# Kernel optimization log

Measured on AMD Instinct MI355X. Metric: run time of the kernel, lower is better.

The kernel has to match this reference:

```python
import jax, jax.numpy as jnp
import numpy as np

B, A, C, M = 4, 120000, 80, 32
ALPHA, GAMMA, EPS = 0.75, 2.0, 1e-4
STD = np.array([0.1, 0.1, 0.2, 0.2, 0.1, 0.1, 0.2, 0.2], dtype=np.float32)


def _make_boxes(key, shape, img=1024.0):
    k1, k2, k3, k4 = jax.random.split(key, 4)
    cx = jax.random.uniform(k1, shape) * img
    cy = jax.random.uniform(k2, shape) * img
    w = jax.random.uniform(k3, shape) * 224.0 + 32.0
    h = jax.random.uniform(k4, shape) * 224.0 + 32.0
    return jnp.stack([cx - 0.5 * w, cy - 0.5 * h, cx + 0.5 * w, cy + 0.5 * h], axis=-1)


def setup_inputs() -> dict:
    key = jax.random.key(0)
    kc, kr, ka, kh, kf, kl, ki = jax.random.split(key, 7)
    classifications = jax.random.uniform(kc, (B, A, C), dtype=jnp.float32)
    regressions = jax.random.normal(kr, (B, A, 8), dtype=jnp.float32)
    anchors = _make_boxes(ka, (1, A))  # [1,A,4]
    head = _make_boxes(kh, (B, M))     # [B,M,4]
    full = _make_boxes(kf, (B, M))     # [B,M,4]
    labels = jax.random.randint(kl, (B, M, 1), 0, C).astype(jnp.float32)
    ignore = jax.random.randint(ki, (B, M, 1), 0, 2).astype(jnp.float32)
    annotations = jnp.concatenate([head, full, labels, ignore], axis=-1)  # [B,M,10]
    return {"classifications": classifications, "regressions": regressions,
            "anchors": anchors, "annotations": annotations}


def _calc_iou(a, b):
    # a: [A,4], b: [B,M,4] -> [B,A,M]
    area_b = (b[..., 2] - b[..., 0]) * (b[..., 3] - b[..., 1])  # [B,M]
    a = a[None, :, None, :]
    bb = b[:, None, :, :]
    iw = jnp.clip(jnp.minimum(a[..., 2], bb[..., 2]) - jnp.maximum(a[..., 0], bb[..., 0]), 0.0)
    ih = jnp.clip(jnp.minimum(a[..., 3], bb[..., 3]) - jnp.maximum(a[..., 1], bb[..., 1]), 0.0)
    area_a = ((a[..., 2] - a[..., 0]) * (a[..., 3] - a[..., 1]))  # [1,A,1]
    inter = iw * ih
    ua = jnp.clip(area_a + area_b[:, None, :] - inter, 1e-8)
    return inter / ua


def reference(classifications, regressions, anchors, annotations):
    anchor = anchors[0]                       # [A,4]
    aw = anchor[:, 2] - anchor[:, 0]
    ah = anchor[:, 3] - anchor[:, 1]
    acx = anchor[:, 0] + 0.5 * aw
    acy = anchor[:, 1] + 0.5 * ah

    ann = annotations[..., :-1]               # [B,M,9]
    full_box = ann[..., 4:8]

    iou = _calc_iou(anchor, full_box)         # [B,A,M]
    iou_max = jnp.max(iou, axis=-1)           # [B,A]
    iou_arg = jnp.argmax(iou, axis=-1)        # [B,A]

    pos = iou_max >= 0.5                      # [B,A]
    neg = iou_max < 0.4
    num_pos = jnp.sum(pos, axis=1).astype(jnp.float32)  # [B]

    assigned = jnp.take_along_axis(ann, iou_arg[..., None], axis=1)  # [B,A,9]
    assigned_cls = assigned[..., 8].astype(jnp.int32)                # [B,A]

    one_hot = jax.nn.one_hot(assigned_cls, classifications.shape[-1], dtype=jnp.float32)
    targets = jnp.where(pos[..., None], one_hot,
                        jnp.where(neg[..., None], 0.0, -1.0))        # [B,A,C]

    p = jnp.clip(classifications, EPS, 1.0 - EPS)
    alpha_f = jnp.where(targets == 1.0, ALPHA, 1.0 - ALPHA)
    focal_w = alpha_f * jnp.where(targets == 1.0, 1.0 - p, p) ** GAMMA
    bce = -(targets * jnp.log(p) + (1.0 - targets) * jnp.log(1.0 - p))
    cls_loss = jnp.where(targets != -1.0, focal_w * bce, 0.0)
    cls_losses = jnp.sum(cls_loss, axis=(1, 2)) / jnp.clip(num_pos, 1.0)  # [B]

    gw_h = assigned[..., 2] - assigned[..., 0]
    gh_h = assigned[..., 3] - assigned[..., 1]
    gcx_h = assigned[..., 0] + 0.5 * gw_h
    gcy_h = assigned[..., 1] + 0.5 * gh_h
    gw_f = assigned[..., 6] - assigned[..., 4]
    gh_f = assigned[..., 7] - assigned[..., 5]
    gcx_f = assigned[..., 4] + 0.5 * gw_f
    gcy_f = assigned[..., 5] + 0.5 * gh_f
    gw_h = jnp.clip(gw_h, 1.0); gh_h = jnp.clip(gh_h, 1.0)
    gw_f = jnp.clip(gw_f, 1.0); gh_f = jnp.clip(gh_f, 1.0)

    t = jnp.stack([
        (gcx_f - acx) / aw, (gcy_f - acy) / ah,
        jnp.log(gw_f / aw), jnp.log(gh_f / ah),
        (gcx_h - acx) / aw * 4.0, (gcy_h - acy) / ah * 4.0,
        jnp.log(gw_h / aw * 4.0), jnp.log(gh_h / ah * 4.0),
    ], axis=-1) / jnp.asarray(STD)            # [B,A,8]

    diff = jnp.abs(t - regressions)
    # only_full=True: weights zero out cols 4:8
    diff = diff * jnp.asarray([1., 1., 1., 1., 0., 0., 0., 0.], dtype=jnp.float32)
    rl = jnp.where(diff <= 1.0 / 9.0, 0.5 * 9.0 * diff * diff, diff - 0.5 / 9.0)
    rl4 = rl[..., 0:4] * pos[..., None]       # [B,A,4], only positive anchors
    reg_losses = jnp.where(num_pos > 0,
                           jnp.sum(rl4, axis=(1, 2)) / (jnp.clip(num_pos, 1.0) * 4.0),
                           0.0)               # mean over positive rows x 4 cols

    return (jnp.mean(cls_losses, keepdims=True), jnp.mean(reg_losses, keepdims=True))
```

## Files before the change

### kernel.cpp

```cpp
#include <hip/hip_runtime.h>

#define NB 4
#define NA 120000
#define NC 80
#define NM 32

#define ALPHA_ 0.75f
#define EPS_   1e-4f
#define LN2_   0.69314718055994531f

constexpr int BLOCK = 192;
constexpr int APB   = 192;
constexpr int F4_PER_ANCHOR = NC / 4;
constexpr int P2_ITERS = APB * F4_PER_ANCHOR / BLOCK;

__device__ __forceinline__ float wave_reduce(float v) {
    #pragma unroll
    for (int off = 32; off > 0; off >>= 1) v += __shfl_down(v, off, 64);
    return v;
}

__device__ __forceinline__ float flog2(float x) { return __builtin_amdgcn_logf(x); }

__global__ __launch_bounds__(BLOCK)
void focal_main(const float* __restrict__ cls,
                const float* __restrict__ reg,
                const float* __restrict__ anchors,
                const float* __restrict__ ann,
                double* __restrict__ acc)
{
    __shared__ float s_ann[NM * 10];
    __shared__ float s_coef[APB];
    __shared__ float s_red[3][3];

    const int b   = blockIdx.y;
    const int a0  = blockIdx.x * APB;
    const int tid = threadIdx.x;

    const float4 an = ((const float4*)anchors)[a0 + tid];

    const float* annB = ann + b * NM * 10;
    const float av0 = annB[tid];
    const float av1 = (tid < NM * 10 - BLOCK) ? annB[BLOCK + tid] : 0.0f;

    const float4* cls4 = (const float4*)(cls + (size_t)b * NA * NC) + (size_t)a0 * F4_PER_ANCHOR;
    float4 x[P2_ITERS];
    #pragma unroll
    for (int it = 0; it < P2_ITERS; ++it)
        x[it] = cls4[it * BLOCK + tid];

    s_ann[tid] = av0;
    if (tid < NM * 10 - BLOCK) s_ann[BLOCK + tid] = av1;
    __syncthreads();

    float regLoss = 0.0f;
    float posCnt  = 0.0f;
    float clsCorr = 0.0f;
    const int a = a0 + tid;

    {
        const float ax1 = an.x, ay1 = an.y, ax2 = an.z, ay2 = an.w;
        const float aw  = ax2 - ax1, ah = ay2 - ay1;
        const float acx = ax1 + 0.5f * aw, acy = ay1 + 0.5f * ah;
        const float areaA = aw * ah;

        float best = -1.0f;
        int   arg  = 0;
        #pragma unroll
        for (int m = 0; m < NM; ++m) {
            const float bx1 = s_ann[m * 10 + 4];
            const float by1 = s_ann[m * 10 + 5];
            const float bx2 = s_ann[m * 10 + 6];
            const float by2 = s_ann[m * 10 + 7];
            float iw = fminf(ax2, bx2) - fmaxf(ax1, bx1); iw = fmaxf(iw, 0.0f);
            float ih = fminf(ay2, by2) - fmaxf(ay1, by1); ih = fmaxf(ih, 0.0f);
            const float inter = iw * ih;
            const float areaB = (bx2 - bx1) * (by2 - by1);
            const float ua    = fmaxf(areaA + areaB - inter, 1e-8f);
            const float iou   = inter / ua;
            if (iou > best) { best = iou; arg = m; }
        }

        const bool pos = best >= 0.5f;
        const bool neg = best < 0.4f;
        s_coef[tid] = (pos || neg) ? (-0.25f * LN2_) : 0.0f;

        if (pos) {
            posCnt = 1.0f;
            const int c = (int)s_ann[arg * 10 + 8];
            const float xc = cls[((size_t)b * NA + a) * NC + c];
            const float p  = fminf(fmaxf(xc, EPS_), 1.0f - EPS_);
            const float q  = 1.0f - p;
            const float posT = 0.75f * q * q * (-LN2_ * flog2(p));
            const float negT = 0.25f * p * p * (-LN2_ * flog2(q));
            clsCorr = posT - negT;

            const float fx1 = s_ann[arg * 10 + 4];
            const float fy1 = s_ann[arg * 10 + 5];
            const float fx2 = s_ann[arg * 10 + 6];
            const float fy2 = s_ann[arg * 10 + 7];
            float gw = fx2 - fx1, gh = fy2 - fy1;
            const float gcx = fx1 + 0.5f * gw, gcy = fy1 + 0.5f * gh;
            gw = fmaxf(gw, 1.0f); gh = fmaxf(gh, 1.0f);
            const float t0 = ((gcx - acx) / aw) * 10.0f;
            const float t1 = ((gcy - acy) / ah) * 10.0f;
            const float t2 = (LN2_ * flog2(gw / aw)) * 5.0f;
            const float t3 = (LN2_ * flog2(gh / ah)) * 5.0f;
            const float4 r4 = ((const float4*)reg)[(size_t)(b * NA + a) * 2];
            const float d0 = fabsf(t0 - r4.x);
            const float d1 = fabsf(t1 - r4.y);
            const float d2 = fabsf(t2 - r4.z);
            const float d3 = fabsf(t3 - r4.w);
            const float beta = 1.0f / 9.0f;
            #define SL1(d) ((d) <= beta ? 4.5f * (d) * (d) : (d) - 0.5f / 9.0f)
            regLoss = SL1(d0) + SL1(d1) + SL1(d2) + SL1(d3);
            #undef SL1
        }
    }
    __syncthreads();

    float clsSum = clsCorr;
    #pragma unroll
    for (int it = 0; it < P2_ITERS; ++it) {
        const int idx = it * BLOCK + tid;
        const float C = s_coef[idx / F4_PER_ANCHOR];
        const float4 x4 = x[it];

        float p0 = fminf(fmaxf(x4.x, EPS_), 1.0f - EPS_);
        float p1 = fminf(fmaxf(x4.y, EPS_), 1.0f - EPS_);
        float p2 = fminf(fmaxf(x4.z, EPS_), 1.0f - EPS_);
        float p3 = fminf(fmaxf(x4.w, EPS_), 1.0f - EPS_);

        float t0 = p0 * p0 * flog2(1.0f - p0);
        float t1 = p1 * p1 * flog2(1.0f - p1);
        float t2 = p2 * p2 * flog2(1.0f - p2);
        float t3 = p3 * p3 * flog2(1.0f - p3);

        clsSum = fmaf((t0 + t1) + (t2 + t3), C, clsSum);
    }

    const int wave = tid >> 6, lane = tid & 63;
    float rc = wave_reduce(clsSum);
    float rr = wave_reduce(regLoss);
    float rp = wave_reduce(posCnt);
    if (lane == 0) { s_red[0][wave] = rc; s_red[1][wave] = rr; s_red[2][wave] = rp; }
    __syncthreads();
    if (tid == 0) {
        float c = s_red[0][0] + s_red[0][1] + s_red[0][2];
        float r = s_red[1][0] + s_red[1][1] + s_red[1][2];
        float p = s_red[2][0] + s_red[2][1] + s_red[2][2];
        atomicAdd(&acc[b * 3 + 0], (double)c);
        atomicAdd(&acc[b * 3 + 1], (double)r);
        atomicAdd(&acc[b * 3 + 2], (double)p);
    }
}

__global__ void focal_finalize(const double* __restrict__ acc, float* __restrict__ out) {
    double clsTot = 0.0, regTot = 0.0;
    #pragma unroll
    for (int b = 0; b < NB; ++b) {
        const double np  = acc[b * 3 + 2];
        const double npc = np < 1.0 ? 1.0 : np;
        clsTot += acc[b * 3 + 0] / npc;
        regTot += (np > 0.0) ? acc[b * 3 + 1] / (npc * 4.0) : 0.0;
    }
    out[0] = (float)(clsTot / NB);
    out[1] = (float)(regTot / NB);
}

extern "C" void kernel_launch(void* const* d_in, const int* in_sizes, int n_in,
                              void* d_out, int out_size, void* d_ws, size_t ws_size,
                              hipStream_t stream) {
    const float* cls     = (const float*)d_in[0];
    const float* reg     = (const float*)d_in[1];
    const float* anchors = (const float*)d_in[2];
    const float* ann     = (const float*)d_in[3];
    float* out = (float*)d_out;
    double* acc = (double*)d_ws;

    hipMemsetAsync(acc, 0, NB * 3 * sizeof(double), stream);

    dim3 grid(NA / APB, NB);
    focal_main<<<grid, BLOCK, 0, stream>>>(cls, reg, anchors, ann, acc);
    focal_finalize<<<1, 1, 0, stream>>>(acc, out);
}
```

Before: 259.0 us.

## Shrink per-block anchor tile, bin global atomics, and parallelize finalize reduction

Blocks now cover 64 anchors with 256 threads, so there are three times as many blocks. Only the first wave does the IoU matching, and all threads load the classification tile after the matching phase. Per-block partial sums go to 64 spread-out atomic bins per accumulator instead of a single address, which cuts atomic contention. The finalize kernel now reduces those bins with wave shuffles across 768 threads. The cls loads no longer overlap the IoU loop inside a block, so the design relies on higher occupancy to hide memory latency.

```diff
diff --git a/kernel.cpp b/kernel.cpp
--- a/kernel.cpp
+++ b/kernel.cpp
@@ -5,16 +5,20 @@
 #define NC 80
 #define NM 32
 
-#define ALPHA_ 0.75f
 #define EPS_   1e-4f
 #define LN2_   0.69314718055994531f
 
-constexpr int BLOCK = 192;
-constexpr int APB   = 192;
-constexpr int F4_PER_ANCHOR = NC / 4;
-constexpr int P2_ITERS = APB * F4_PER_ANCHOR / BLOCK;
+constexpr int BLOCK = 256;
+constexpr int APB   = 64;
+constexpr int U     = 5;
+constexpr int BINS  = 64;
 
-__device__ __forceinline__ float wave_reduce(float v) {
+__device__ __forceinline__ float wave_reduce_f(float v) {
+    #pragma unroll
+    for (int off = 32; off > 0; off >>= 1) v += __shfl_down(v, off, 64);
+    return v;
+}
+__device__ __forceinline__ double wave_reduce_d(double v) {
     #pragma unroll
     for (int off = 32; off > 0; off >>= 1) v += __shfl_down(v, off, 64);
     return v;
@@ -23,42 +27,33 @@
 __device__ __forceinline__ float flog2(float x) { return __builtin_amdgcn_logf(x); }
 
 __global__ __launch_bounds__(BLOCK)
-void focal_main(const float* __restrict__ cls,
-                const float* __restrict__ reg,
-                const float* __restrict__ anchors,
-                const float* __restrict__ ann,
-                double* __restrict__ acc)
+void focal_fused(const float* __restrict__ cls,
+                 const float* __restrict__ reg,
+                 const float* __restrict__ anchors,
+                 const float* __restrict__ ann,
+                 double* __restrict__ acc)
 {
     __shared__ float s_ann[NM * 10];
     __shared__ float s_coef[APB];
-    __shared__ float s_red[3][3];
+    __shared__ float s_red[4];
+    __shared__ float s_rp[2];
 
     const int b   = blockIdx.y;
     const int a0  = blockIdx.x * APB;
     const int tid = threadIdx.x;
 
-    const float4 an = ((const float4*)anchors)[a0 + tid];
-
     const float* annB = ann + b * NM * 10;
-    const float av0 = annB[tid];
-    const float av1 = (tid < NM * 10 - BLOCK) ? annB[BLOCK + tid] : 0.0f;
-
-    const float4* cls4 = (const float4*)(cls + (size_t)b * NA * NC) + (size_t)a0 * F4_PER_ANCHOR;
-    float4 x[P2_ITERS];
-    #pragma unroll
-    for (int it = 0; it < P2_ITERS; ++it)
-        x[it] = cls4[it * BLOCK + tid];
-
-    s_ann[tid] = av0;
-    if (tid < NM * 10 - BLOCK) s_ann[BLOCK + tid] = av1;
+    if (tid < NM * 10 - BLOCK) s_ann[BLOCK + tid] = annB[BLOCK + tid];
+    s_ann[tid] = annB[tid];
     __syncthreads();
 
     float regLoss = 0.0f;
     float posCnt  = 0.0f;
     float clsCorr = 0.0f;
-    const int a = a0 + tid;
 
-    {
+    if (tid < APB) {
+        const int a = a0 + tid;
+        const float4 an = ((const float4*)anchors)[a];
         const float ax1 = an.x, ay1 = an.y, ax2 = an.z, ay2 = an.w;
         const float aw  = ax2 - ax1, ah = ay2 - ay1;
         const float acx = ax1 + 0.5f * aw, acy = ay1 + 0.5f * ah;
@@ -119,12 +114,19 @@
     }
     __syncthreads();
 
+    const float4* base4 = (const float4*)(cls + (size_t)b * NA * NC) + (size_t)a0 * (NC / 4);
+
+    float4 x[U];
+    #pragma unroll
+    for (int j = 0; j < U; ++j)
+        x[j] = base4[j * BLOCK + tid];
+
     float clsSum = clsCorr;
     #pragma unroll
-    for (int it = 0; it < P2_ITERS; ++it) {
-        const int idx = it * BLOCK + tid;
-        const float C = s_coef[idx / F4_PER_ANCHOR];
-        const float4 x4 = x[it];
+    for (int j = 0; j < U; ++j) {
+        const int idx = j * BLOCK + tid;
+        const float C = s_coef[idx / (NC / 4)];
+        const float4 x4 = x[j];
 
         float p0 = fminf(fmaxf(x4.x, EPS_), 1.0f - EPS_);
         float p1 = fminf(fmaxf(x4.y, EPS_), 1.0f - EPS_);
@@ -140,32 +142,43 @@
     }
 
     const int wave = tid >> 6, lane = tid & 63;
-    float rc = wave_reduce(clsSum);
-    float rr = wave_reduce(regLoss);
-    float rp = wave_reduce(posCnt);
-    if (lane == 0) { s_red[0][wave] = rc; s_red[1][wave] = rr; s_red[2][wave] = rp; }
+    float rc = wave_reduce_f(clsSum);
+    if (lane == 0) s_red[wave] = rc;
+    if (wave == 0) {
+        float rr = wave_reduce_f(regLoss);
+        float rp = wave_reduce_f(posCnt);
+        if (lane == 0) { s_rp[0] = rr; s_rp[1] = rp; }
+    }
     __syncthreads();
     if (tid == 0) {
-        float c = s_red[0][0] + s_red[0][1] + s_red[0][2];
-        float r = s_red[1][0] + s_red[1][1] + s_red[1][2];
-        float p = s_red[2][0] + s_red[2][1] + s_red[2][2];
-        atomicAdd(&acc[b * 3 + 0], (double)c);
-        atomicAdd(&acc[b * 3 + 1], (double)r);
-        atomicAdd(&acc[b * 3 + 2], (double)p);
+        const float c = (s_red[0] + s_red[1]) + (s_red[2] + s_red[3]);
+        const int bin = blockIdx.x & (BINS - 1);
+        atomicAdd(&acc[(b * 3 + 0) * BINS + bin], (double)c);
+        atomicAdd(&acc[(b * 3 + 1) * BINS + bin], (double)s_rp[0]);
+        atomicAdd(&acc[(b * 3 + 2) * BINS + bin], (double)s_rp[1]);
     }
 }
 
 __global__ void focal_finalize(const double* __restrict__ acc, float* __restrict__ out) {
-    double clsTot = 0.0, regTot = 0.0;
-    #pragma unroll
-    for (int b = 0; b < NB; ++b) {
-        const double np  = acc[b * 3 + 2];
-        const double npc = np < 1.0 ? 1.0 : np;
-        clsTot += acc[b * 3 + 0] / npc;
-        regTot += (np > 0.0) ? acc[b * 3 + 1] / (npc * 4.0) : 0.0;
+    __shared__ double g[NB * 3];
+    const int tid  = threadIdx.x;
+    const int wave = tid >> 6, lane = tid & 63;
+    double v = acc[wave * BINS + lane];
+    v = wave_reduce_d(v);
+    if (lane == 0) g[wave] = v;
+    __syncthreads();
+    if (tid == 0) {
+        double clsTot = 0.0, regTot = 0.0;
+        #pragma unroll
+        for (int b = 0; b < NB; ++b) {
+            const double np  = g[b * 3 + 2];
+            const double npc = np < 1.0 ? 1.0 : np;
+            clsTot += g[b * 3 + 0] / npc;
+            regTot += (np > 0.0) ? g[b * 3 + 1] / (npc * 4.0) : 0.0;
+        }
+        out[0] = (float)(clsTot / NB);
+        out[1] = (float)(regTot / NB);
     }
-    out[0] = (float)(clsTot / NB);
-    out[1] = (float)(regTot / NB);
 }
 
 extern "C" void kernel_launch(void* const* d_in, const int* in_sizes, int n_in,
@@ -178,9 +191,9 @@
     float* out = (float*)d_out;
     double* acc = (double*)d_ws;
 
-    hipMemsetAsync(acc, 0, NB * 3 * sizeof(double), stream);
+    hipMemsetAsync(acc, 0, NB * 3 * BINS * sizeof(double), stream);
 
     dim3 grid(NA / APB, NB);
-    focal_main<<<grid, BLOCK, 0, stream>>>(cls, reg, anchors, ann, acc);
-    focal_finalize<<<1, 1, 0, stream>>>(acc, out);
+    focal_fused<<<grid, BLOCK, 0, stream>>>(cls, reg, anchors, ann, acc);
+    focal_finalize<<<1, NB * 3 * BINS, 0, stream>>>(acc, out);
 }
```

Result: faster. 235.9 us (-8.9%).
